# Kernel tuning notes

Measured on AMD Instinct MI355X. Metric: run time of the kernel, lower is better.

## Reference

```python
import jax, jax.numpy as jnp
import numpy as np

NUM_CLASSES = 21
IGNORE_INDEX = 0
BN_EPS = 1e-5
VAR_EPS = 1e-6
NORM_EPS = 1e-12


def _class_stats(feat, onehot, counts):
    # feat: (B, C, P)  onehot: (B, P, K)  counts: (B, K)
    sums = jnp.einsum('bcp,bpk->bkc', feat, onehot)          # (B, K, C)
    sumsq = jnp.einsum('bcp,bpk->bkc', feat * feat, onehot)  # (B, K, C)
    cnt = counts[:, :, None]
    cnt_safe = jnp.maximum(cnt, 1.0)
    mu = sums / cnt_safe
    # unbiased variance, matching torch .var(dim=1) default
    denom = jnp.maximum(cnt - 1.0, 1.0)
    var = (sumsq - cnt * mu * mu) / denom + VAR_EPS
    return mu, var


def _l2_normalize(x):
    # F.normalize(x, p=2, dim=1): x / max(||x||_2, eps)
    n = jnp.sqrt(jnp.sum(x * x, axis=1, keepdims=True))
    return x / jnp.maximum(n, NORM_EPS)


def _ppa_forward(s_feat, t_feat, gt, W_proj, gamma, beta):
    # proj_s: 1x1 conv (no bias) + BatchNorm2d (training-mode batch stats) + ReLU
    x = jnp.einsum('bchw,oc->bohw', s_feat, W_proj)
    m = x.mean(axis=(0, 2, 3), keepdims=True)
    v = x.var(axis=(0, 2, 3), keepdims=True)  # biased, as BN uses
    x = (x - m) / jnp.sqrt(v + BN_EPS)
    x = x * gamma[None, :, None, None] + beta[None, :, None, None]
    s = jnp.maximum(x, 0.0)

    t = jax.lax.stop_gradient(t_feat)  # t_feat.detach()
    s = _l2_normalize(s)
    t = _l2_normalize(t)

    mse_total = jnp.mean((s - t) ** 2)

    B, C, H, W = s.shape
    P = H * W
    s_flat = s.reshape(B, C, P)
    t_flat = t.reshape(B, C, P)
    mask_flat = gt.reshape(B, P)

    onehot = jax.nn.one_hot(mask_flat, NUM_CLASSES, dtype=s.dtype)  # (B, P, K)
    counts = onehot.sum(axis=1)                                      # (B, K)

    mu_s, var_s = _class_stats(s_flat, onehot, counts)
    mu_t, var_t = _class_stats(t_flat, onehot, counts)

    # class valid iff count > 1 and class != ignore_index (same for s and t)
    class_ids = jnp.arange(NUM_CLASSES)
    valid = (counts > 1.0) & (class_ids[None, :] != IGNORE_INDEX)    # (B, K)

    loss_mu = jnp.mean((mu_s - mu_t) ** 2, axis=-1)    # (B, K)
    loss_var = jnp.mean((var_s - var_t) ** 2, axis=-1)  # (B, K)
    mm = 0.5 * loss_mu + 0.5 * loss_var

    cnt = jnp.sum(valid.astype(s.dtype))
    loss = jnp.sum(jnp.where(valid, mm, 0.0)) / (cnt + 1e-7)
    return loss + 0.5 * mse_total


def setup_inputs() -> dict:
    key = jax.random.key(0)
    k1, k2, k3, k4 = jax.random.split(key, 4)
    B, H, W = 8, 128, 128
    s_feat = jax.random.normal(k1, (B, 320, H, W), dtype=jnp.float32)
    t_feat = jax.random.normal(k2, (B, 256, H, W), dtype=jnp.float32)
    gt = jax.random.randint(k3, (B, H, W), 0, NUM_CLASSES)
    W_proj = jax.random.normal(k4, (256, 320), dtype=jnp.float32) * 0.05
    gamma = jnp.ones((256,), dtype=jnp.float32)
    beta = jnp.zeros((256,), dtype=jnp.float32)
    return {"s_feat": s_feat, "t_feat": t_feat, "gt": gt,
            "W_proj": W_proj, "gamma": gamma, "beta": beta}


def reference(s_feat, t_feat, gt, W_proj, gamma, beta):
    return _ppa_forward(s_feat, t_feat, gt, W_proj, gamma, beta)
```

## Files before the change

kernel.cpp:

```cpp
#include <hip/hip_runtime.h>
#include <hip/hip_bf16.h>

typedef unsigned short u16;
typedef __attribute__((ext_vector_type(2))) unsigned short us2;
typedef __attribute__((ext_vector_type(4))) float          f32x4;
typedef __attribute__((ext_vector_type(8))) short          bf8;
typedef __attribute__((ext_vector_type(8))) unsigned short us8;
typedef __attribute__((ext_vector_type(4))) unsigned short us4;

#define BATCH 8
#define CIN   320
#define COUT  256
#define NPIX  16384
#define NCLS  21
#define KCLS  32
#define MTOT  (BATCH*NPIX)
#define SROW  320
#define TSTR  66

__device__ __forceinline__ float bf2f(u16 v){
    unsigned int u = ((unsigned int)v) << 16;
    float f; __builtin_memcpy(&f, &u, 4); return f;
}
__device__ __forceinline__ u16 f2bf(float f){
    __hip_bfloat16 h = __float2bfloat16(f);
    u16 r; __builtin_memcpy(&r, &h, 2); return r;
}

__global__ void k0_wcvt(const float* __restrict__ W, u16* __restrict__ Wbf, float* __restrict__ zbuf){
    int i4 = blockIdx.x * 256 + threadIdx.x;
    float4 v = reinterpret_cast<const float4*>(W)[i4];
    us4 o;
    o[0] = f2bf(v.x); o[1] = f2bf(v.y); o[2] = f2bf(v.z); o[3] = f2bf(v.w);
    reinterpret_cast<us4*>(Wbf)[i4] = o;
    if (blockIdx.x == 0){
        for (int i = threadIdx.x; i < 832; i += 256) zbuf[i] = 0.f;
    }
}

__global__ __launch_bounds__(256) void kt_strans(const float* __restrict__ in, u16* __restrict__ out){
    __shared__ float tile[64*65];
    const int t  = threadIdx.x;
    const int bid = blockIdx.x;
    const int pt = bid & 255;
    const int ct = (bid >> 8) % 5;
    const int b  = bid / (256*5);
    const float* src = in + ((size_t)b*CIN + ct*64)*NPIX + pt*64;
    #pragma unroll
    for (int it = 0; it < 4; it++){
        int f = it*256 + t;
        int i = f >> 4, c4 = f & 15;
        float4 v = *reinterpret_cast<const float4*>(src + (size_t)i*NPIX + c4*4);
        float* d = &tile[i*65 + c4*4];
        d[0]=v.x; d[1]=v.y; d[2]=v.z; d[3]=v.w;
    }
    __syncthreads();
    u16* dst = out + ((size_t)(b*NPIX + pt*64))*SROW + ct*64;
    #pragma unroll
    for (int it = 0; it < 2; it++){
        int f = it*256 + t;
        int p = f >> 3, c8 = f & 7;
        us8 o;
        #pragma unroll
        for (int j = 0; j < 8; j++) o[j] = f2bf(tile[(c8*8+j)*65 + p]);
        *reinterpret_cast<us8*>(dst + (size_t)p*SROW + c8*8) = o;
    }
}

__global__ __launch_bounds__(256, 2) void k1_mfma(u16* SX, const u16* __restrict__ Wbf,
                                                  float* __restrict__ bnsum, float* __restrict__ bnsumsq){
    __shared__ __align__(16) char sm[67584];
    __shared__ float bns[512];
    const int t = threadIdx.x;
    const int wid = t >> 6, l = t & 63;
    const size_t pblk = (size_t)blockIdx.x * 128;
    const int wm = (wid & 1) * 64;
    const int wn = (wid >> 1) * 128;
    bns[t] = 0.f; bns[t+256] = 0.f;

    f32x4 acc[4][8];
    #pragma unroll
    for (int mi = 0; mi < 4; mi++)
        #pragma unroll
        for (int ni = 0; ni < 8; ni++)
            acc[mi][ni] = (f32x4){0.f,0.f,0.f,0.f};

    const int sg = t & 7, sp = t >> 3;
    const u16* srcb = SX + (pblk + sp) * SROW + sg * 8;
    us8 stg[4];
    #pragma unroll
    for (int it = 0; it < 4; it++)
        stg[it] = *reinterpret_cast<const us8*>(srcb + (size_t)it*32*SROW);

    for (int kt = 0; kt < 5; kt++){
        __syncthreads();
        #pragma unroll
        for (int it = 0; it < 4; it++){
            int p = sp + it*32;
            int byt = p*128 + ((sg*16) ^ ((p&7)<<4));
            *reinterpret_cast<us8*>(&sm[byt]) = stg[it];
        }
        if (kt < 4){
            #pragma unroll
            for (int it = 0; it < 4; it++)
                stg[it] = *reinterpret_cast<const us8*>(srcb + (size_t)it*32*SROW + (kt+1)*64);
        }
        __syncthreads();
        #pragma unroll
        for (int ks = 0; ks < 2; ks++){
            bf8 bfr[8], afr[4];
            const u16* wp = Wbf + (size_t)(wn + (l & 15)) * CIN + kt*64 + ks*32 + (l >> 4)*8;
            #pragma unroll
            for (int ni = 0; ni < 8; ni++)
                bfr[ni] = *reinterpret_cast<const bf8*>(wp + (size_t)ni*16*CIN);
            #pragma unroll
            for (int mi = 0; mi < 4; mi++){
                int p = wm + mi*16 + (l & 15);
                int byt = p*128 + (((ks*4 + (l>>4))*16) ^ ((p&7)<<4));
                afr[mi] = *reinterpret_cast<const bf8*>(&sm[byt]);
            }
            #pragma unroll
            for (int mi = 0; mi < 4; mi++)
                #pragma unroll
                for (int ni = 0; ni < 8; ni++)
                    acc[mi][ni] = __builtin_amdgcn_mfma_f32_16x16x32_bf16(afr[mi], bfr[ni], acc[mi][ni], 0, 0, 0);
        }
    }
    __syncthreads();
    #pragma unroll
    for (int mi = 0; mi < 4; mi++)
        #pragma unroll
        for (int ni = 0; ni < 8; ni++)
            #pragma unroll
            for (int r = 0; r < 4; r++){
                int p = wm + mi*16 + (l>>4)*4 + r;
                int o = wn + ni*16 + (l&15);
                *reinterpret_cast<u16*>(&sm[(p*264 + o)*2]) = f2bf(acc[mi][ni][r]);
            }
    __syncthreads();
    float s1[8], s2[8];
    #pragma unroll
    for (int j = 0; j < 8; j++){ s1[j] = 0.f; s2[j] = 0.f; }
    const int oc = (t & 31) * 8;
    const int pr = t >> 5;
    #pragma unroll
    for (int it = 0; it < 16; it++){
        int p = pr + it*8;
        us8 v = *reinterpret_cast<const us8*>(&sm[(p*264 + oc)*2]);
        *reinterpret_cast<us8*>(SX + (pblk + p)*SROW + oc) = v;
        #pragma unroll
        for (int j = 0; j < 8; j++){
            float fv = bf2f(v[j]);
            s1[j] += fv; s2[j] += fv*fv;
        }
    }
    #pragma unroll
    for (int j = 0; j < 8; j++){
        atomicAdd(&bns[oc + j],       s1[j]);
        atomicAdd(&bns[256 + oc + j], s2[j]);
    }
    __syncthreads();
    atomicAdd(&bnsum[t],   bns[t]);
    atomicAdd(&bnsumsq[t], bns[t + 256]);
}

__global__ void k2_bn(const float* __restrict__ bnsum, const float* __restrict__ bnsumsq,
                      const float* __restrict__ gamma, const float* __restrict__ beta,
                      float* __restrict__ bna, float* __restrict__ bnb){
    int o = threadIdx.x;
    float m = bnsum[o] / (float)MTOT;
    float v = bnsumsq[o] / (float)MTOT - m * m;
    float a = gamma[o] / sqrtf(v + 1e-5f);
    bna[o] = a;
    bnb[o] = beta[o] - m * a;
}

__global__ void k3_counts(const int* __restrict__ gt, float* __restrict__ counts){
    __shared__ float h[NCLS];
    const int b = blockIdx.x >> 5, seg = blockIdx.x & 31, t = threadIdx.x;
    if (t < NCLS) h[t] = 0.f;
    __syncthreads();
    const int* g = gt + b * NPIX + seg * 512;
    for (int i = t; i < 512; i += 256) atomicAdd(&h[g[i]], 1.0f);
    __syncthreads();
    if (t < NCLS) atomicAdd(&counts[b * NCLS + t], h[t]);
}

__global__ __launch_bounds__(512, 2) void k4_fused(u16* SX, const float* __restrict__ T,
                                                   const int* __restrict__ gt,
                                                   const float* __restrict__ bna, const float* __restrict__ bnb,
                                                   float* __restrict__ msep){
    __shared__ u16 tsb[256*TSTR];
    __shared__ u16 sbb[256*TSTR];
    __shared__ float nt_l[64];
    __shared__ float rt_l[64];
    __shared__ int   gtile[64];
    __shared__ float msw[8];
    const int t = threadIdx.x, wid = t >> 6, l = t & 63;
    const int b  = blockIdx.x >> 6;
    const int pb = (blockIdx.x & 63) * 256;
    const float a0=bna[l], a1=bna[l+64], a2=bna[l+128], a3=bna[l+192];
    const float c0=bnb[l], c1=bnb[l+64], c2=bnb[l+128], c3=bnb[l+192];
    const float* Tb = T + (size_t)b * COUT * NPIX;
    const int* gtb = gt + b * NPIX;
    const u16* Xb = SX + (size_t)b * NPIX * SROW;
    float msea = 0.f;

    f32x4 acc[4][2][2];
    #pragma unroll
    for (int ty = 0; ty < 4; ty++)
        #pragma unroll
        for (int sl = 0; sl < 2; sl++)
            #pragma unroll
            for (int hf = 0; hf < 2; hf++)
                acc[ty][sl][hf] = (f32x4){0.f,0.f,0.f,0.f};

    const int sc4 = t >> 4, sp4 = t & 15;
    f32x4 pstg[8];
    int gstg = 0;
    {
        #pragma unroll
        for (int it = 0; it < 8; it++)
            pstg[it] = *reinterpret_cast<const f32x4*>(Tb + (size_t)(it*32 + sc4)*NPIX + pb + sp4*4);
        if (t < 64) gstg = gtb[pb + t];
    }

    for (int tile = 0; tile < 4; tile++){
        const int q0 = pb + tile*64;
        if (t < 64) nt_l[t] = 0.f;
        __syncthreads();
        {
            float nq0=0.f, nq1=0.f, nq2=0.f, nq3=0.f;
            #pragma unroll
            for (int it = 0; it < 8; it++){
                int c = it*32 + sc4;
                f32x4 v = pstg[it];
                nq0 += v[0]*v[0]; nq1 += v[1]*v[1]; nq2 += v[2]*v[2]; nq3 += v[3]*v[3];
                int base = c*TSTR + sp4*4;
                us2 w0; w0[0] = f2bf(v[0]); w0[1] = f2bf(v[1]);
                us2 w1; w1[0] = f2bf(v[2]); w1[1] = f2bf(v[3]);
                *reinterpret_cast<us2*>(&tsb[base])     = w0;
                *reinterpret_cast<us2*>(&tsb[base + 2]) = w1;
            }
            atomicAdd(&nt_l[sp4*4+0], nq0);
            atomicAdd(&nt_l[sp4*4+1], nq1);
            atomicAdd(&nt_l[sp4*4+2], nq2);
            atomicAdd(&nt_l[sp4*4+3], nq3);
            if (t < 64) gtile[t] = gstg;
        }
        if (tile < 3){
            const int q1 = q0 + 64;
            #pragma unroll
            for (int it = 0; it < 8; it++)
                pstg[it] = *reinterpret_cast<const f32x4*>(Tb + (size_t)(it*32 + sc4)*NPIX + q1 + sp4*4);
            if (t < 64) gstg = gtb[q1 + t];
        }
        __syncthreads();
        if (t < 64) rt_l[t] = 1.0f / fmaxf(sqrtf(nt_l[t]), 1e-12f);
        #pragma unroll
        for (int u = 0; u < 8; u++){
            int pxl = wid*8 + u;
            const u16* xr = Xb + (size_t)(q0 + pxl) * SROW;
            float s0 = fmaxf(fmaf(a0, bf2f(xr[l]),     c0), 0.f);
            float s1 = fmaxf(fmaf(a1, bf2f(xr[l+64]),  c1), 0.f);
            float s2 = fmaxf(fmaf(a2, bf2f(xr[l+128]), c2), 0.f);
            float s3 = fmaxf(fmaf(a3, bf2f(xr[l+192]), c3), 0.f);
            float ns = s0*s0 + s1*s1 + s2*s2 + s3*s3;
            #pragma unroll
            for (int off = 32; off; off >>= 1) ns += __shfl_xor(ns, off, 64);
            float rs = 1.0f / fmaxf(sqrtf(ns), 1e-12f);
            sbb[(l      )*TSTR + pxl] = f2bf(s0*rs);
            sbb[(l + 64 )*TSTR + pxl] = f2bf(s1*rs);
            sbb[(l + 128)*TSTR + pxl] = f2bf(s2*rs);
            sbb[(l + 192)*TSTR + pxl] = f2bf(s3*rs);
        }
        __syncthreads();
        #pragma unroll
        for (int ks = 0; ks < 2; ks++){
            const int px0 = ks*32 + (l>>4)*8;
            bf8 aA0, aA1;
            #pragma unroll
            for (int j = 0; j < 8; j++){
                int gv = gtile[px0 + j];
                aA0[j] = (short)((gv == (l & 15))      ? 0x3F80 : 0);
                aA1[j] = (short)((gv == (l & 15) + 16) ? 0x3F80 : 0);
            }
            float rtj[8];
            #pragma unroll
            for (int q = 0; q < 4; q++){
                float2 rv = *reinterpret_cast<const float2*>(&rt_l[px0 + 2*q]);
                rtj[2*q] = rv.x; rtj[2*q+1] = rv.y;
            }
            #pragma unroll
            for (int sl = 0; sl < 2; sl++){
                const int cw = wid*16 + (l & 15) + sl*128;
                const int tbase = cw*TSTR + px0;
                bf8 bS, bS2, bT, bT2;
                #pragma unroll
                for (int q = 0; q < 4; q++){
                    us2 tv = *reinterpret_cast<const us2*>(&tsb[tbase + 2*q]);
                    us2 sv = *reinterpret_cast<const us2*>(&sbb[tbase + 2*q]);
                    #pragma unroll
                    for (int e = 0; e < 2; e++){
                        int j = 2*q + e;
                        float ft = bf2f(tv[e]) * rtj[j];
                        float fs = bf2f(sv[e]);
                        bT[j]  = (short)f2bf(ft);
                        bT2[j] = (short)f2bf(ft*ft);
                        bS[j]  = (short)sv[e];
                        bS2[j] = (short)f2bf(fs*fs);
                        float d = fs - ft;
                        msea += d*d;
                    }
                }
                acc[0][sl][0] = __builtin_amdgcn_mfma_f32_16x16x32_bf16(aA0, bS,  acc[0][sl][0], 0,0,0);
                acc[0][sl][1] = __builtin_amdgcn_mfma_f32_16x16x32_bf16(aA1, bS,  acc[0][sl][1], 0,0,0);
                acc[1][sl][0] = __builtin_amdgcn_mfma_f32_16x16x32_bf16(aA0, bS2, acc[1][sl][0], 0,0,0);
                acc[1][sl][1] = __builtin_amdgcn_mfma_f32_16x16x32_bf16(aA1, bS2, acc[1][sl][1], 0,0,0);
                acc[2][sl][0] = __builtin_amdgcn_mfma_f32_16x16x32_bf16(aA0, bT,  acc[2][sl][0], 0,0,0);
                acc[2][sl][1] = __builtin_amdgcn_mfma_f32_16x16x32_bf16(aA1, bT,  acc[2][sl][1], 0,0,0);
                acc[3][sl][0] = __builtin_amdgcn_mfma_f32_16x16x32_bf16(aA0, bT2, acc[3][sl][0], 0,0,0);
                acc[3][sl][1] = __builtin_amdgcn_mfma_f32_16x16x32_bf16(aA1, bT2, acc[3][sl][1], 0,0,0);
            }
        }
    }

    {
        u16* Pb = SX + (size_t)blockIdx.x * 256 * SROW;
        #pragma unroll
        for (int ty = 0; ty < 4; ty++)
            #pragma unroll
            for (int sl = 0; sl < 2; sl++)
                #pragma unroll
                for (int hf = 0; hf < 2; hf++)
                    #pragma unroll
                    for (int r = 0; r < 4; r++){
                        int k = hf*16 + (l>>4)*4 + r;
                        int c = wid*16 + (l & 15) + sl*128;
                        int i = (ty*KCLS + k)*COUT + c;
                        Pb[(size_t)(i >> 7)*SROW + (i & 127)] = f2bf(acc[ty][sl][hf][r]);
                    }
    }
    #pragma unroll
    for (int off = 32; off; off >>= 1) msea += __shfl_xor(msea, off, 64);
    if (l == 0) msw[wid] = msea;
    __syncthreads();
    if (t == 0){
        float v = 0.f;
        #pragma unroll
        for (int i = 0; i < 8; i++) v += msw[i];
        atomicAdd(msep, v);
    }
}

__global__ void kR_reduce(const u16* __restrict__ SX,
                          float* __restrict__ gss, float* __restrict__ gsq,
                          float* __restrict__ gts, float* __restrict__ gtq){
    int g = blockIdx.x * 256 + threadIdx.x;
    #pragma unroll
    for (int it = 0; it < 4; it++, g += 65536){
        int i  = g & 32767;
        int b  = g >> 15;
        float s = 0.f;
        #pragma unroll
        for (int sl = 0; sl < 64; sl++){
            const u16* p = SX + ((size_t)((b*64 + sl)*256 + (i >> 7)))*SROW + (i & 127);
            s += bf2f(*p);
        }
        int ty = i >> 13;
        int kc = i & 8191;
        float* G = (ty==0)? gss : (ty==1)? gsq : (ty==2)? gts : gtq;
        G[b*8192 + kc] = s;
    }
}

__global__ void kA_pairs(const float* __restrict__ counts,
                         const float* __restrict__ gs,  const float* __restrict__ gqs,
                         const float* __restrict__ gtm, const float* __restrict__ gqt,
                         float* __restrict__ mmacc, float* __restrict__ ccacc){
    __shared__ float red[4];
    const int bk = blockIdx.x;
    const int b = bk / NCLS, k = bk - b*NCLS;
    const int t = threadIdx.x, wid = t >> 6, l = t & 63;
    const float cnt = counts[bk];
    const float cs = fmaxf(cnt, 1.f);
    const float dn = fmaxf(cnt - 1.f, 1.f);
    const int idx = (b*KCLS + k)*COUT + t;
    float mus = gs[idx] / cs;
    float vas = (gqs[idx] - cnt*mus*mus) / dn + 1e-6f;
    float mut = gtm[idx] / cs;
    float vat = (gqt[idx] - cnt*mut*mut) / dn + 1e-6f;
    float dm = mus - mut, dv = vas - vat;
    float a = dm*dm + dv*dv;
    #pragma unroll
    for (int off = 32; off; off >>= 1) a += __shfl_xor(a, off, 64);
    if (l == 0) red[wid] = a;
    __syncthreads();
    if (t == 0 && cnt > 1.f && k != 0){
        atomicAdd(mmacc, 0.5f * (red[0]+red[1]+red[2]+red[3]) / (float)COUT);
        atomicAdd(ccacc, 1.f);
    }
}

__global__ void kB_final(const float* __restrict__ mmacc, const float* __restrict__ ccacc,
                         const float* __restrict__ msep, float* __restrict__ out){
    out[0] = mmacc[0] / (ccacc[0] + 1e-7f) + 0.5f * (msep[0] / (float)((size_t)MTOT * COUT));
}

extern "C" void kernel_launch(void* const* d_in, const int* in_sizes, int n_in,
                              void* d_out, int out_size, void* d_ws, size_t ws_size,
                              hipStream_t stream){
    (void)in_sizes; (void)n_in; (void)out_size; (void)ws_size;
    const float* s_feat = (const float*)d_in[0];
    const float* t_feat = (const float*)d_in[1];
    const int*   gt     = (const int*)d_in[2];
    const float* Wp     = (const float*)d_in[3];
    const float* gamma  = (const float*)d_in[4];
    const float* beta   = (const float*)d_in[5];
    char* ws = (char*)d_ws;

    u16*   SX   = (u16*)ws;
    u16*   Wbf  = (u16*)(ws + 83886080);
    char*  z0   = ws + 84049920;
    float* bnsum    = (float*)(z0);
    float* bnsumsq  = (float*)(z0 + 1024);
    float* msep     = (float*)(z0 + 2048);
    float* mmacc    = (float*)(z0 + 2064);
    float* ccacc    = (float*)(z0 + 2080);
    float* counts   = (float*)(z0 + 2304);
    float* bna      = (float*)(z0 + 3328);
    float* bnb      = (float*)(z0 + 4352);
    float* gsum_s   = (float*)(z0 + 5376);
    float* gsumsq_s = (float*)(z0 + 5376 + 262144);
    float* gsum_t   = (float*)(z0 + 5376 + 2*262144);
    float* gsumsq_t = (float*)(z0 + 5376 + 3*262144);


    k0_wcvt  <<<80,    256, 0, stream>>>(Wp, Wbf, (float*)z0);
    kt_strans<<<10240, 256, 0, stream>>>(s_feat, SX);
    k1_mfma  <<<1024,  256, 0, stream>>>(SX, Wbf, bnsum, bnsumsq);
    k2_bn    <<<1,     256, 0, stream>>>(bnsum, bnsumsq, gamma, beta, bna, bnb);
    k3_counts<<<256,   256, 0, stream>>>(gt, counts);
    k4_fused <<<512,   512, 0, stream>>>(SX, t_feat, gt, bna, bnb, msep);
    kR_reduce<<<256,   256, 0, stream>>>(SX, gsum_s, gsumsq_s, gsum_t, gsumsq_t);
    kA_pairs <<<168,   256, 0, stream>>>(counts, gsum_s, gsumsq_s, gsum_t, gsumsq_t, mmacc, ccacc);
    kB_final <<<1,     1,   0, stream>>>(mmacc, ccacc, msep, (float*)d_out);
}
```

Before: 223.5 us.

## Fold BN finalize into fused kernel and read teacher features from global

Removes the single-block BN-finalize kernel launch and has each k4_fused thread compute its BN scale and shift directly from the accumulated sums, gamma and beta. It also drops the bf16 teacher tile staged in shared memory: the T values are re-read from global (expected to hit cache) inside the MFMA loop and used in full fp32 precision. This halves the kernel's LDS footprint, which may let more blocks be resident, and removes one launch. The cost is redundant BN math per block and extra global loads for teacher data.

```diff
diff --git a/kernel.cpp b/kernel.cpp
--- a/kernel.cpp
+++ b/kernel.cpp
@@ -164,17 +164,6 @@
     atomicAdd(&bnsumsq[t], bns[t + 256]);
 }
 
-__global__ void k2_bn(const float* __restrict__ bnsum, const float* __restrict__ bnsumsq,
-                      const float* __restrict__ gamma, const float* __restrict__ beta,
-                      float* __restrict__ bna, float* __restrict__ bnb){
-    int o = threadIdx.x;
-    float m = bnsum[o] / (float)MTOT;
-    float v = bnsumsq[o] / (float)MTOT - m * m;
-    float a = gamma[o] / sqrtf(v + 1e-5f);
-    bna[o] = a;
-    bnb[o] = beta[o] - m * a;
-}
-
 __global__ void k3_counts(const int* __restrict__ gt, float* __restrict__ counts){
     __shared__ float h[NCLS];
     const int b = blockIdx.x >> 5, seg = blockIdx.x & 31, t = threadIdx.x;
@@ -188,9 +177,9 @@
 
 __global__ __launch_bounds__(512, 2) void k4_fused(u16* SX, const float* __restrict__ T,
                                                    const int* __restrict__ gt,
-                                                   const float* __restrict__ bna, const float* __restrict__ bnb,
+                                                   const float* __restrict__ bnsum, const float* __restrict__ bnsumsq,
+                                                   const float* __restrict__ gamma, const float* __restrict__ beta,
                                                    float* __restrict__ msep){
-    __shared__ u16 tsb[256*TSTR];
     __shared__ u16 sbb[256*TSTR];
     __shared__ float nt_l[64];
     __shared__ float rt_l[64];
@@ -199,8 +188,18 @@
     const int t = threadIdx.x, wid = t >> 6, l = t & 63;
     const int b  = blockIdx.x >> 6;
     const int pb = (blockIdx.x & 63) * 256;
-    const float a0=bna[l], a1=bna[l+64], a2=bna[l+128], a3=bna[l+192];
-    const float c0=bnb[l], c1=bnb[l+64], c2=bnb[l+128], c3=bnb[l+192];
+    const float inv = 1.0f / (float)MTOT;
+    float a0, a1, a2, a3, c0, c1, c2, c3;
+    {
+        float m0 = bnsum[l      ]*inv, v0 = bnsumsq[l      ]*inv - m0*m0;
+        float m1 = bnsum[l + 64 ]*inv, v1 = bnsumsq[l + 64 ]*inv - m1*m1;
+        float m2 = bnsum[l + 128]*inv, v2 = bnsumsq[l + 128]*inv - m2*m2;
+        float m3 = bnsum[l + 192]*inv, v3 = bnsumsq[l + 192]*inv - m3*m3;
+        a0 = gamma[l      ] / sqrtf(v0 + 1e-5f); c0 = beta[l      ] - m0*a0;
+        a1 = gamma[l + 64 ] / sqrtf(v1 + 1e-5f); c1 = beta[l + 64 ] - m1*a1;
+        a2 = gamma[l + 128] / sqrtf(v2 + 1e-5f); c2 = beta[l + 128] - m2*a2;
+        a3 = gamma[l + 192] / sqrtf(v3 + 1e-5f); c3 = beta[l + 192] - m3*a3;
+    }
     const float* Tb = T + (size_t)b * COUT * NPIX;
     const int* gtb = gt + b * NPIX;
     const u16* Xb = SX + (size_t)b * NPIX * SROW;
@@ -233,14 +232,8 @@
             float nq0=0.f, nq1=0.f, nq2=0.f, nq3=0.f;
             #pragma unroll
             for (int it = 0; it < 8; it++){
-                int c = it*32 + sc4;
                 f32x4 v = pstg[it];
                 nq0 += v[0]*v[0]; nq1 += v[1]*v[1]; nq2 += v[2]*v[2]; nq3 += v[3]*v[3];
-                int base = c*TSTR + sp4*4;
-                us2 w0; w0[0] = f2bf(v[0]); w0[1] = f2bf(v[1]);
-                us2 w1; w1[0] = f2bf(v[2]); w1[1] = f2bf(v[3]);
-                *reinterpret_cast<us2*>(&tsb[base])     = w0;
-                *reinterpret_cast<us2*>(&tsb[base + 2]) = w1;
             }
             atomicAdd(&nt_l[sp4*4+0], nq0);
             atomicAdd(&nt_l[sp4*4+1], nq1);
@@ -294,16 +287,19 @@
             #pragma unroll
             for (int sl = 0; sl < 2; sl++){
                 const int cw = wid*16 + (l & 15) + sl*128;
-                const int tbase = cw*TSTR + px0;
+                const float* tg = Tb + (size_t)cw*NPIX + q0 + px0;
+                f32x4 ta = *reinterpret_cast<const f32x4*>(tg);
+                f32x4 tb4 = *reinterpret_cast<const f32x4*>(tg + 4);
+                const int sbase = cw*TSTR + px0;
                 bf8 bS, bS2, bT, bT2;
                 #pragma unroll
                 for (int q = 0; q < 4; q++){
-                    us2 tv = *reinterpret_cast<const us2*>(&tsb[tbase + 2*q]);
-                    us2 sv = *reinterpret_cast<const us2*>(&sbb[tbase + 2*q]);
+                    us2 sv = *reinterpret_cast<const us2*>(&sbb[sbase + 2*q]);
                     #pragma unroll
                     for (int e = 0; e < 2; e++){
                         int j = 2*q + e;
-                        float ft = bf2f(tv[e]) * rtj[j];
+                        float traw = (j < 4) ? ta[j] : tb4[j-4];
+                        float ft = traw * rtj[j];
                         float fs = bf2f(sv[e]);
                         bT[j]  = (short)f2bf(ft);
                         bT2[j] = (short)f2bf(ft*ft);
@@ -428,8 +424,6 @@
     float* mmacc    = (float*)(z0 + 2064);
     float* ccacc    = (float*)(z0 + 2080);
     float* counts   = (float*)(z0 + 2304);
-    float* bna      = (float*)(z0 + 3328);
-    float* bnb      = (float*)(z0 + 4352);
     float* gsum_s   = (float*)(z0 + 5376);
     float* gsumsq_s = (float*)(z0 + 5376 + 262144);
     float* gsum_t   = (float*)(z0 + 5376 + 2*262144);
@@ -439,9 +433,8 @@
     k0_wcvt  <<<80,    256, 0, stream>>>(Wp, Wbf, (float*)z0);
     kt_strans<<<10240, 256, 0, stream>>>(s_feat, SX);
     k1_mfma  <<<1024,  256, 0, stream>>>(SX, Wbf, bnsum, bnsumsq);
-    k2_bn    <<<1,     256, 0, stream>>>(bnsum, bnsumsq, gamma, beta, bna, bnb);
     k3_counts<<<256,   256, 0, stream>>>(gt, counts);
-    k4_fused <<<512,   512, 0, stream>>>(SX, t_feat, gt, bna, bnb, msep);
+    k4_fused <<<512,   512, 0, stream>>>(SX, t_feat, gt, bnsum, bnsumsq, gamma, beta, msep);
     kR_reduce<<<256,   256, 0, stream>>>(SX, gsum_s, gsumsq_s, gsum_t, gsumsq_t);
     kA_pairs <<<168,   256, 0, stream>>>(counts, gsum_s, gsumsq_s, gsum_t, gsumsq_t, mmacc, ccacc);
     kB_final <<<1,     1,   0, stream>>>(mmacc, ccacc, msep, (float*)d_out);
```

After: 227.2 us. Within noise of the previous version (+1.7%).
